# Kernel optimization log

Hardware: AMD Instinct MI355X
Metric: run time of the kernel (lower is better)

The kernel has to match this reference:

```python
import jax, jax.numpy as jnp
import numpy as np
from jax import lax

B, N, T = 64, 50, 30          # batch, history length, words per title
VOCAB, E = 50000, 300          # vocab size, word emb dim
FN, A, G, K = 400, 200, 400, 3 # filter_num, attention_dim, gru_unit, window size
USERS = 50000


def setup_inputs() -> dict:
    key = jax.random.key(0)
    ks = jax.random.split(key, 12)
    return {
        "user_id": jax.random.randint(ks[0], (B,), 0, USERS),
        "history_title": jax.random.randint(ks[1], (B, N, T), 0, VOCAB),
        "history_length": jax.random.randint(ks[2], (B,), 1, N + 1),
        "word_emb": jax.random.normal(ks[3], (VOCAB, E), jnp.float32) * 0.02,
        "conv_w": jax.random.normal(ks[4], (K, E, FN), jnp.float32) * 0.05,  # WIO layout
        "conv_b": jnp.zeros((FN,), jnp.float32),
        "v": jax.random.normal(ks[5], (FN, A), jnp.float32) * 0.05,
        "vb": jnp.zeros((A,), jnp.float32),
        "q": jax.random.normal(ks[6], (A, 1), jnp.float32) * 0.05,
        "user_emb": jax.random.normal(ks[7], (USERS, G), jnp.float32) * 0.02,
        "W_ih": jax.random.normal(ks[8], (3 * G, FN), jnp.float32) * 0.05,
        "W_hh": jax.random.normal(ks[9], (3 * G, G), jnp.float32) * 0.05,
        "b_ih": jnp.zeros((3 * G,), jnp.float32),
        "b_hh": jnp.zeros((3 * G,), jnp.float32),
    }


def _news_encode(history_title, word_emb, conv_w, conv_b, v, vb, q):
    # word embedding lookup: [B, N, T, E] (dropout is identity in eval mode)
    W = word_emb[history_title]
    # Conv1d over the word axis, padding=1 keeps length T
    x = W.reshape(B * N, T, E)
    C = lax.conv_general_dilated(
        x, conv_w, window_strides=(1,), padding=[(1, 1)],
        dimension_numbers=("NWC", "WIO", "NWC")) + conv_b
    C = jax.nn.relu(C).reshape(B, N, T, FN)
    # additive attention scores
    a = jnp.tanh(jnp.einsum("bntf,fa->bnta", C, v) + vb)
    a = jnp.einsum("bnta,ao->bnt", a, q)  # q: [A,1] -> squeeze
    # original uses Softmax(dim=0) on a [n, t] per sample => over the n-titles axis
    alpha = jax.nn.softmax(a, axis=1)
    # e[i] = alpha[i] @ C[i]: weighted sum over words -> [B, N, FN]
    return jnp.einsum("bnt,bntf->bnf", alpha, C)


def _gru(news_embed, h0, lengths, W_ih, W_hh, b_ih, b_hh):
    # packed_padded semantics: h stops updating once step >= length
    xs = jnp.swapaxes(news_embed, 0, 1)                 # [N, B, FN]
    mask = jnp.arange(N)[:, None] < lengths[None, :]    # [N, B]

    def step(h, inp):
        x_t, m = inp
        gx = x_t @ W_ih.T + b_ih                        # [B, 3G]
        gh = h @ W_hh.T + b_hh
        xr, xz, xn = jnp.split(gx, 3, axis=-1)
        hr, hz, hn = jnp.split(gh, 3, axis=-1)
        r = jax.nn.sigmoid(xr + hr)
        z = jax.nn.sigmoid(xz + hz)
        n = jnp.tanh(xn + r * hn)
        h_new = (1.0 - z) * n + z * h
        h = jnp.where(m[:, None], h_new, h)
        return h, None

    h_final, _ = lax.scan(step, h0, (xs, mask))
    return h_final


def reference(user_id, history_title, history_length, word_emb, conv_w, conv_b,
              v, vb, q, user_emb, W_ih, W_hh, b_ih, b_hh):
    news_embed = _news_encode(history_title, word_emb, conv_w, conv_b, v, vb, q)
    h0 = user_emb[user_id]                              # [B, G]
    return _gru(news_embed, h0, history_length, W_ih, W_hh, b_ih, b_hh)
```

## Files before the change

### kernel.cpp

```cpp
#include <hip/hip_runtime.h>
#include <hip/hip_bf16.h>

#define BB 64
#define NN 50
#define TT 30
#define EE 300
#define FN 400
#define AA 200
#define GG 400

typedef __attribute__((ext_vector_type(8))) short bf16x8;
typedef __attribute__((ext_vector_type(4))) float f32x4;

__device__ inline ushort f2bf(float x) {
  __hip_bfloat16 b = __float2bfloat16(x);
  return *(ushort*)&b;
}

__global__ void k_prep_all(
    const float* __restrict__ Whh, const float* __restrict__ cw,
    const float* __restrict__ v, const float* __restrict__ q,
    const float* __restrict__ vb, const float* __restrict__ Wih,
    const int* __restrict__ user_id, const float* __restrict__ user_emb,
    float* __restrict__ Wpack, __hip_bfloat16* __restrict__ WT2,
    __hip_bfloat16* __restrict__ vT, float* __restrict__ qp,
    float* __restrict__ vbp, __hip_bfloat16* __restrict__ Wih_bf,
    float* __restrict__ h0)
{
  int i = blockIdx.x * 256 + threadIdx.x;
  if (i < 480000) {
    int jl = i % 150;
    int g = (i / 150) % 400;
    int gc = i / 60000;
    int gate = jl / 50, gl = jl - gate * 50;
    int j = gate * 400 + gc * 50 + gl;
    Wpack[i] = Whh[j * 400 + g];
  } else if (i < 910080) {
    int k = i - 480000;
    int kk = k & 31, f = (k >> 5) % 448, s = k / (448 * 32);
    int ko = s / 10, e = (s - ko * 10) * 32 + kk;
    float val = (f < FN && e < EE) ? cw[(ko * EE + e) * FN + f] : 0.f;
    WT2[k] = __float2bfloat16(val);
  } else if (i < 1003264) {
    int k = i - 910080;
    int a = k / 416, f = k % 416;
    vT[k] = __float2bfloat16((a < AA && f < FN) ? v[f * AA + a] : 0.f);
  } else if (i < 1003488) {
    int k = i - 1003264;
    qp[k]  = k < AA ? q[k]  : 0.f;
    vbp[k] = k < AA ? vb[k] : 0.f;
  } else if (i < 1562592) {
    int k = i - 1003488;
    int j = k / 416, f = k % 416;
    Wih_bf[k] = __float2bfloat16((j < 1200 && f < FN) ? Wih[j * 400 + f] : 0.f);
  } else if (i < 1588192) {
    int k = i - 1562592;
    int b = k / GG, g = k - b * GG;
    h0[k] = user_emb[(size_t)user_id[b] * GG + g];
  }
}

__global__ __launch_bounds__(512, 4) void k_conv(
    const int* __restrict__ title, const float* __restrict__ word_emb,
    const __hip_bfloat16* __restrict__ WT2, const float* __restrict__ conv_b,
    __hip_bfloat16* __restrict__ C)
{
  __shared__ __align__(16) ushort E[2][34][340];
  __shared__ int words[60];
  const int g = blockIdx.x;
  const int tid = threadIdx.x;
  const int lane = tid & 63, wid = tid >> 6;
  const int ti = wid >> 2, wn = wid & 3;
  const int l15 = lane & 15, l4 = lane >> 4;

  if (tid < 60) words[tid] = title[g * 60 + tid];
  for (int idx = tid; idx < 2890; idx += 512)
    *(uint4*)((ushort*)E + idx * 8) = make_uint4(0u, 0u, 0u, 0u);
  __syncthreads();
  for (int idx = tid; idx < 4500; idx += 512) {
    int row = idx / 75, ch = idx - row * 75;
    int tt = row / 30, w = row - tt * 30;
    float4 v4 = *(const float4*)(word_emb + (size_t)words[row] * EE + ch * 4);
    ushort4 u4 = make_ushort4(f2bf(v4.x), f2bf(v4.y), f2bf(v4.z), f2bf(v4.w));
    *(ushort4*)(&E[tt][w + 1][ch * 4]) = u4;
  }
  __syncthreads();

  f32x4 acc[2][7];
#pragma unroll
  for (int nt = 0; nt < 7; ++nt) {
    int f = wn * 112 + nt * 16 + l15;
    float bj = (f < FN) ? conv_b[f] : 0.f;
#pragma unroll
    for (int mt = 0; mt < 2; ++mt) {
      acc[mt][nt][0] = bj; acc[mt][nt][1] = bj;
      acc[mt][nt][2] = bj; acc[mt][nt][3] = bj;
    }
  }

  const ushort* Bbase = (const ushort*)WT2 + (size_t)(wn * 112 + l15) * 32 + l4 * 8;

#pragma unroll
  for (int ko = 0; ko < 3; ++ko) {
#pragma unroll
    for (int ks = 0; ks < 10; ++ks) {
      const int s = ko * 10 + ks;
      bf16x8 bq[7];
#pragma unroll
      for (int nt = 0; nt < 7; ++nt)
        bq[nt] = *(const bf16x8*)(Bbase + (size_t)s * 14336 + nt * 512);
      bf16x8 af[2];
#pragma unroll
      for (int mt = 0; mt < 2; ++mt)
        af[mt] = *(const bf16x8*)(&E[ti][mt * 16 + l15 + ko][ks * 32 + l4 * 8]);
#pragma unroll
      for (int nt = 0; nt < 7; ++nt)
#pragma unroll
        for (int mt = 0; mt < 2; ++mt)
          acc[mt][nt] = __builtin_amdgcn_mfma_f32_16x16x32_bf16(af[mt], bq[nt], acc[mt][nt], 0, 0, 0);
    }
  }

#pragma unroll
  for (int mt = 0; mt < 2; ++mt) {
    int tb = mt * 16 + l4 * 4;
#pragma unroll
    for (int nt = 0; nt < 7; ++nt) {
      int f = wn * 112 + nt * 16 + l15;
      if (f < 416) {
#pragma unroll
        for (int r = 0; r < 4; ++r) {
          int t = tb + r;
          if (t < TT) {
            float vv = fmaxf(acc[mt][nt][r], 0.f);
            C[((size_t)(g * 2 + ti) * 30 + t) * 416 + f] = __float2bfloat16(vv);
          }
        }
      }
    }
  }
}

__global__ __launch_bounds__(512) void k_attn(
    const __hip_bfloat16* __restrict__ C, const __hip_bfloat16* __restrict__ vT,
    const float* __restrict__ vbp, const float* __restrict__ qp,
    float* __restrict__ score)
{
  __shared__ __align__(16) ushort Clds[256 * 40];
  __shared__ __align__(16) ushort Vlds[224 * 40];
  __shared__ float sred[2][256];
  const int tid = threadIdx.x;
  const int lane = tid & 63, wid = tid >> 6;
  const int wm = wid >> 1, wn = wid & 1;
  const int l15 = lane & 15, l4 = lane >> 4;
  const size_t row0 = (size_t)blockIdx.x * 256;

  f32x4 acc[4][7];
  float ql[7];
#pragma unroll
  for (int nt = 0; nt < 7; ++nt) {
    int a = wn * 112 + nt * 16 + l15;
    ql[nt] = qp[a];
    float vbv = vbp[a];
#pragma unroll
    for (int mt = 0; mt < 4; ++mt) {
      acc[mt][nt][0] = vbv; acc[mt][nt][1] = vbv;
      acc[mt][nt][2] = vbv; acc[mt][nt][3] = vbv;
    }
  }

  for (int ks = 0; ks < 13; ++ks) {
    for (int idx = tid; idx < 1024; idx += 512) {
      int r = idx >> 2, c = idx & 3;
      *(uint4*)(&Clds[r * 40 + c * 8]) =
          *(const uint4*)((const ushort*)C + (row0 + r) * 416 + ks * 32 + c * 8);
    }
    for (int idx = tid; idx < 896; idx += 512) {
      int a = idx >> 2, c = idx & 3;
      *(uint4*)(&Vlds[a * 40 + c * 8]) =
          *(const uint4*)((const ushort*)vT + a * 416 + ks * 32 + c * 8);
    }
    __syncthreads();
    bf16x8 cf[4];
#pragma unroll
    for (int mt = 0; mt < 4; ++mt)
      cf[mt] = *(const bf16x8*)(&Clds[(wm * 64 + mt * 16 + l15) * 40 + l4 * 8]);
#pragma unroll
    for (int nt = 0; nt < 7; ++nt) {
      bf16x8 vf = *(const bf16x8*)(&Vlds[(wn * 112 + nt * 16 + l15) * 40 + l4 * 8]);
#pragma unroll
      for (int mt = 0; mt < 4; ++mt)
        acc[mt][nt] = __builtin_amdgcn_mfma_f32_16x16x32_bf16(cf[mt], vf, acc[mt][nt], 0, 0, 0);
    }
    __syncthreads();
  }

  float sums[4][4];
#pragma unroll
  for (int mt = 0; mt < 4; ++mt)
#pragma unroll
    for (int r = 0; r < 4; ++r) sums[mt][r] = 0.f;
#pragma unroll
  for (int mt = 0; mt < 4; ++mt)
#pragma unroll
    for (int nt = 0; nt < 7; ++nt)
#pragma unroll
      for (int r = 0; r < 4; ++r)
        sums[mt][r] += tanhf(acc[mt][nt][r]) * ql[nt];
#pragma unroll
  for (int mask = 1; mask < 16; mask <<= 1)
#pragma unroll
    for (int mt = 0; mt < 4; ++mt)
#pragma unroll
      for (int r = 0; r < 4; ++r)
        sums[mt][r] += __shfl_xor(sums[mt][r], mask);

  float outv = 0.f;
#pragma unroll
  for (int mt = 0; mt < 4; ++mt)
#pragma unroll
    for (int r = 0; r < 4; ++r)
      if (l15 == mt * 4 + r) outv = sums[mt][r];
  sred[wn][wm * 64 + (l15 >> 2) * 16 + l4 * 4 + (l15 & 3)] = outv;
  __syncthreads();
  if (tid < 256) score[row0 + tid] = sred[0][tid] + sred[1][tid];
}

__global__ void k2_softmax_n(const float* __restrict__ score, float* __restrict__ alpha) {
  int i = blockIdx.x * 256 + threadIdx.x;
  if (i >= BB * TT) return;
  int b = i / TT, t = i - b * TT;
  int base = b * (NN * TT) + t;
  float m = -1e30f;
  for (int n = 0; n < NN; ++n) m = fmaxf(m, score[base + n * TT]);
  float s = 0.f;
  for (int n = 0; n < NN; ++n) s += __expf(score[base + n * TT] - m);
  float inv = 1.f / s;
  for (int n = 0; n < NN; ++n)
    alpha[base + n * TT] = __expf(score[base + n * TT] - m) * inv;
}

__global__ __launch_bounds__(256) void k3_wsum(
    const float* __restrict__ alpha, const __hip_bfloat16* __restrict__ C,
    __hip_bfloat16* __restrict__ Ebf) {
  __shared__ float al[TT];
  const int bn = blockIdx.x;
  const int tid = threadIdx.x;
  if (tid < TT) al[tid] = alpha[bn * TT + tid];
  __syncthreads();
  for (int f = tid; f < 416; f += 256) {
    float s = 0.f;
    if (f < FN) {
#pragma unroll
      for (int t = 0; t < TT; ++t)
        s = fmaf(al[t], __bfloat162float(C[((size_t)bn * TT + t) * 416 + f]), s);
    }
    Ebf[(size_t)bn * 416 + f] = __float2bfloat16(s);
  }
}

__global__ __launch_bounds__(512) void k4_gx_mfma(
    const __hip_bfloat16* __restrict__ Ebf,
    const __hip_bfloat16* __restrict__ Wih,
    const float* __restrict__ b_ih,
    float* __restrict__ gx)
{
  __shared__ __align__(16) ushort Alds[128 * 40];
  __shared__ __align__(16) ushort Blds[448 * 40];
  const int tid = threadIdx.x;
  const int lane = tid & 63, wid = tid >> 6;
  const int wm = wid >> 2, wn = wid & 3;
  const int l15 = lane & 15, l4 = lane >> 4;
  const int mb = blockIdx.x / 3;
  const int nb = blockIdx.x - mb * 3;
  const int row0 = mb * 128;
  const int n0 = nb * 448;

  f32x4 acc[4][7];
#pragma unroll
  for (int nt = 0; nt < 7; ++nt) {
    int j = n0 + wn * 112 + nt * 16 + l15;
    float bj = (j < 1200) ? b_ih[j] : 0.f;
#pragma unroll
    for (int mt = 0; mt < 4; ++mt) {
      acc[mt][nt][0] = bj; acc[mt][nt][1] = bj;
      acc[mt][nt][2] = bj; acc[mt][nt][3] = bj;
    }
  }

  const int ar = tid >> 2, ac = tid & 3;
  for (int ks = 0; ks < 13; ++ks) {
    *(uint4*)(&Alds[ar * 40 + ac * 8]) =
        *(const uint4*)((const ushort*)Ebf + (size_t)(row0 + ar) * 416 + ks * 32 + ac * 8);
    for (int idx = tid; idx < 1792; idx += 512) {
      int r = idx >> 2, c = idx & 3;
      *(uint4*)(&Blds[r * 40 + c * 8]) =
          *(const uint4*)((const ushort*)Wih + (size_t)(n0 + r) * 416 + ks * 32 + c * 8);
    }
    __syncthreads();
    bf16x8 af[4];
#pragma unroll
    for (int mt = 0; mt < 4; ++mt)
      af[mt] = *(const bf16x8*)(&Alds[(wm * 64 + mt * 16 + l15) * 40 + l4 * 8]);
#pragma unroll
    for (int nt = 0; nt < 7; ++nt) {
      bf16x8 bfr = *(const bf16x8*)(&Blds[(wn * 112 + nt * 16 + l15) * 40 + l4 * 8]);
#pragma unroll
      for (int mt = 0; mt < 4; ++mt)
        acc[mt][nt] = __builtin_amdgcn_mfma_f32_16x16x32_bf16(af[mt], bfr, acc[mt][nt], 0, 0, 0);
    }
    __syncthreads();
  }

#pragma unroll
  for (int mt = 0; mt < 4; ++mt) {
    int row = row0 + wm * 64 + mt * 16 + l4 * 4;
#pragma unroll
    for (int nt = 0; nt < 7; ++nt) {
      int j = n0 + wn * 112 + nt * 16 + l15;
      if (j < 1200) {
#pragma unroll
        for (int r = 0; r < 4; ++r)
          gx[(size_t)(row + r) * 1200 + j] = acc[mt][nt][r];
      }
    }
  }
}

__global__ __launch_bounds__(256) void k5_step(
    const float* __restrict__ h_prev, float* __restrict__ h_next,
    const float* __restrict__ Wpack, const float* __restrict__ b_hh,
    const float* __restrict__ gx, const int* __restrict__ hist_len,
    float* __restrict__ out, int step)
{
  const int gc = blockIdx.x & 7;
  const int bg = blockIdx.x >> 3;
  const int tid = threadIdx.x;
  __shared__ float hl[2][GG];
  __shared__ float ghl[2][3][50];

  for (int i = tid; i < 2 * GG; i += 256) {
    int b = i / GG, g = i - b * GG;
    hl[b][g] = h_prev[(2 * bg + b) * GG + g];
  }
  __syncthreads();

  if (tid < 150) {
    float a00 = 0.f, a01 = 0.f, a10 = 0.f, a11 = 0.f;
    const float* wp = Wpack + (size_t)gc * 60000 + tid;
#pragma unroll 4
    for (int g = 0; g < 200; ++g) {
      float w0 = wp[g * 150];
      float w1 = wp[(g + 200) * 150];
      a00 = fmaf(hl[0][g], w0, a00);
      a10 = fmaf(hl[1][g], w0, a10);
      a01 = fmaf(hl[0][g + 200], w1, a01);
      a11 = fmaf(hl[1][g + 200], w1, a11);
    }
    int gate = tid / 50, gl = tid - gate * 50;
    float bb = b_hh[gate * 400 + gc * 50 + gl];
    ghl[0][gate][gl] = a00 + a01 + bb;
    ghl[1][gate][gl] = a10 + a11 + bb;
  }
  __syncthreads();

  if (tid < 100) {
    int b = tid / 50, gl = tid - (tid / 50) * 50;
    int babs = 2 * bg + b;
    int g = gc * 50 + gl;
    const float* gxp = gx + ((size_t)babs * NN + step) * 1200;
    float xr = gxp[g], xz = gxp[400 + g], xn = gxp[800 + g];
    float hr = ghl[b][0][gl], hz = ghl[b][1][gl], hn = ghl[b][2][gl];
    float r = 1.f / (1.f + __expf(-(xr + hr)));
    float z = 1.f / (1.f + __expf(-(xz + hz)));
    float nv = tanhf(xn + r * hn);
    float hold = hl[b][g];
    float hnew = (1.f - z) * nv + z * hold;
    float hres = (step < hist_len[babs]) ? hnew : hold;
    h_next[babs * GG + g] = hres;
    if (step == NN - 1) out[babs * GG + g] = hres;
  }
}

extern "C" void kernel_launch(void* const* d_in, const int* in_sizes, int n_in,
                              void* d_out, int out_size, void* d_ws, size_t ws_size,
                              hipStream_t stream) {
  const int*   user_id   = (const int*)d_in[0];
  const int*   title     = (const int*)d_in[1];
  const int*   hist_len  = (const int*)d_in[2];
  const float* word_emb  = (const float*)d_in[3];
  const float* conv_w    = (const float*)d_in[4];
  const float* conv_b    = (const float*)d_in[5];
  const float* v         = (const float*)d_in[6];
  const float* vb        = (const float*)d_in[7];
  const float* q         = (const float*)d_in[8];
  const float* user_emb  = (const float*)d_in[9];
  const float* W_ih      = (const float*)d_in[10];
  const float* W_hh      = (const float*)d_in[11];
  const float* b_ih      = (const float*)d_in[12];
  const float* b_hh      = (const float*)d_in[13];
  float* out = (float*)d_out;

  char* ws = (char*)d_ws;
  size_t off = 0;
  auto take = [&](size_t bytes) {
    char* p = ws + off;
    off = (off + bytes + 255) & ~(size_t)255;
    return p;
  };
  __hip_bfloat16* C      = (__hip_bfloat16*)take((size_t)BB * NN * TT * 416 * 2);
  float* score  = (float*)take((size_t)BB * NN * TT * 4);
  float* alpha  = (float*)take((size_t)BB * NN * TT * 4);
  __hip_bfloat16* Ebf    = (__hip_bfloat16*)take((size_t)BB * NN * 416 * 2);
  __hip_bfloat16* Wih_bf = (__hip_bfloat16*)take((size_t)1344 * 416 * 2);
  float* Wpack  = (float*)take((size_t)8 * 400 * 150 * 4);
  float* gx     = (float*)take((size_t)BB * NN * 1200 * 4);
  float* h0     = (float*)take((size_t)BB * GG * 4);
  float* h1     = (float*)take((size_t)BB * GG * 4);
  __hip_bfloat16* WT2    = (__hip_bfloat16*)take((size_t)30 * 448 * 32 * 2);
  __hip_bfloat16* vT     = (__hip_bfloat16*)take((size_t)224 * 416 * 2);
  float* qp     = (float*)take(224 * 4);
  float* vbp    = (float*)take(224 * 4);
  (void)ws_size;

  k_prep_all<<<6204, 256, 0, stream>>>(W_hh, conv_w, v, q, vb, W_ih, user_id,
                                       user_emb, Wpack, WT2, vT, qp, vbp,
                                       Wih_bf, h0);

  k_conv<<<BB * NN / 2, 512, 0, stream>>>(title, word_emb, WT2, conv_b, C);
  k_attn<<<BB * NN * TT / 256, 512, 0, stream>>>(C, vT, vbp, qp, score);
  k2_softmax_n<<<(BB * TT + 255) / 256, 256, 0, stream>>>(score, alpha);
  k3_wsum<<<BB * NN, 256, 0, stream>>>(alpha, C, Ebf);
  k4_gx_mfma<<<75, 512, 0, stream>>>(Ebf, Wih_bf, b_ih, gx);

  float* hbuf[2] = {h0, h1};
  for (int step = 0; step < NN; ++step) {
    k5_step<<<256, 256, 0, stream>>>(hbuf[step & 1], hbuf[(step + 1) & 1],
                                     Wpack, b_hh, gx, hist_len, out, step);
  }
}
```

Measured before the change: 894.5 us.

## Reuse conv weight fragments across both titles and stream V weights directly from global

Result: no change. 882.0 us (-1.4%).

```diff
diff --git a/kernel.cpp b/kernel.cpp
--- a/kernel.cpp
+++ b/kernel.cpp
@@ -23,7 +23,7 @@
     const float* __restrict__ vb, const float* __restrict__ Wih,
     const int* __restrict__ user_id, const float* __restrict__ user_emb,
     float* __restrict__ Wpack, __hip_bfloat16* __restrict__ WT2,
-    __hip_bfloat16* __restrict__ vT, float* __restrict__ qp,
+    __hip_bfloat16* __restrict__ vT2, float* __restrict__ qp,
     float* __restrict__ vbp, __hip_bfloat16* __restrict__ Wih_bf,
     float* __restrict__ h0)
 {
@@ -43,8 +43,10 @@
     WT2[k] = __float2bfloat16(val);
   } else if (i < 1003264) {
     int k = i - 910080;
-    int a = k / 416, f = k % 416;
-    vT[k] = __float2bfloat16((a < AA && f < FN) ? v[f * AA + a] : 0.f);
+    int kk = k & 31, a = (k >> 5) % 224, ks = k / (224 * 32);
+    int e = ks * 32 + kk;
+    float val = (a < AA && e < FN) ? v[e * AA + a] : 0.f;
+    vT2[k] = __float2bfloat16(val);
   } else if (i < 1003488) {
     int k = i - 1003264;
     qp[k]  = k < AA ? q[k]  : 0.f;
@@ -60,24 +62,23 @@
   }
 }
 
-__global__ __launch_bounds__(512, 4) void k_conv(
+__global__ __launch_bounds__(256, 2) void k_conv(
     const int* __restrict__ title, const float* __restrict__ word_emb,
     const __hip_bfloat16* __restrict__ WT2, const float* __restrict__ conv_b,
     __hip_bfloat16* __restrict__ C)
 {
-  __shared__ __align__(16) ushort E[2][34][340];
+  __shared__ __align__(16) ushort E[2][34][344];
   __shared__ int words[60];
   const int g = blockIdx.x;
   const int tid = threadIdx.x;
-  const int lane = tid & 63, wid = tid >> 6;
-  const int ti = wid >> 2, wn = wid & 3;
+  const int lane = tid & 63, wn = tid >> 6;
   const int l15 = lane & 15, l4 = lane >> 4;
 
   if (tid < 60) words[tid] = title[g * 60 + tid];
-  for (int idx = tid; idx < 2890; idx += 512)
+  for (int idx = tid; idx < 2924; idx += 256)
     *(uint4*)((ushort*)E + idx * 8) = make_uint4(0u, 0u, 0u, 0u);
   __syncthreads();
-  for (int idx = tid; idx < 4500; idx += 512) {
+  for (int idx = tid; idx < 4500; idx += 256) {
     int row = idx / 75, ch = idx - row * 75;
     int tt = row / 30, w = row - tt * 30;
     float4 v4 = *(const float4*)(word_emb + (size_t)words[row] * EE + ch * 4);
@@ -86,13 +87,13 @@
   }
   __syncthreads();
 
-  f32x4 acc[2][7];
+  f32x4 acc[4][7];
 #pragma unroll
   for (int nt = 0; nt < 7; ++nt) {
     int f = wn * 112 + nt * 16 + l15;
     float bj = (f < FN) ? conv_b[f] : 0.f;
 #pragma unroll
-    for (int mt = 0; mt < 2; ++mt) {
+    for (int mt = 0; mt < 4; ++mt) {
       acc[mt][nt][0] = bj; acc[mt][nt][1] = bj;
       acc[mt][nt][2] = bj; acc[mt][nt][3] = bj;
     }
@@ -100,30 +101,43 @@
 
   const ushort* Bbase = (const ushort*)WT2 + (size_t)(wn * 112 + l15) * 32 + l4 * 8;
 
-#pragma unroll
-  for (int ko = 0; ko < 3; ++ko) {
-#pragma unroll
-    for (int ks = 0; ks < 10; ++ks) {
-      const int s = ko * 10 + ks;
-      bf16x8 bq[7];
-#pragma unroll
-      for (int nt = 0; nt < 7; ++nt)
-        bq[nt] = *(const bf16x8*)(Bbase + (size_t)s * 14336 + nt * 512);
-      bf16x8 af[2];
-#pragma unroll
-      for (int mt = 0; mt < 2; ++mt)
-        af[mt] = *(const bf16x8*)(&E[ti][mt * 16 + l15 + ko][ks * 32 + l4 * 8]);
-#pragma unroll
-      for (int nt = 0; nt < 7; ++nt)
-#pragma unroll
-        for (int mt = 0; mt < 2; ++mt)
-          acc[mt][nt] = __builtin_amdgcn_mfma_f32_16x16x32_bf16(af[mt], bq[nt], acc[mt][nt], 0, 0, 0);
-    }
-  }
-
-#pragma unroll
-  for (int mt = 0; mt < 2; ++mt) {
-    int tb = mt * 16 + l4 * 4;
+#define LOADB(dst, s) {                                                        \
+    const ushort* p_ = Bbase + (size_t)(s) * 14336;                            \
+    _Pragma("unroll")                                                          \
+    for (int nt = 0; nt < 7; ++nt) dst[nt] = *(const bf16x8*)(p_ + nt * 512);  \
+  }
+#define DOMFMA(bq, s) {                                                        \
+    const int ko_ = (s) / 10, ks_ = (s) % 10;                                  \
+    bf16x8 af_[4];                                                             \
+    _Pragma("unroll")                                                          \
+    for (int mt = 0; mt < 4; ++mt)                                             \
+      af_[mt] = *(const bf16x8*)(&E[mt >> 1][(mt & 1) * 16 + l15 + ko_]        \
+                                   [ks_ * 32 + l4 * 8]);                       \
+    _Pragma("unroll")                                                          \
+    for (int nt = 0; nt < 7; ++nt)                                             \
+      _Pragma("unroll")                                                        \
+      for (int mt = 0; mt < 4; ++mt)                                           \
+        acc[mt][nt] = __builtin_amdgcn_mfma_f32_16x16x32_bf16(                 \
+            af_[mt], bq[nt], acc[mt][nt], 0, 0, 0);                            \
+  }
+
+  bf16x8 bqA[7], bqB[7];
+  LOADB(bqA, 0);
+#pragma unroll
+  for (int it = 0; it < 15; ++it) {
+    const int s0 = it * 2;
+    LOADB(bqB, s0 + 1);
+    DOMFMA(bqA, s0);
+    if (it < 14) LOADB(bqA, s0 + 2);
+    DOMFMA(bqB, s0 + 1);
+  }
+#undef LOADB
+#undef DOMFMA
+
+#pragma unroll
+  for (int mt = 0; mt < 4; ++mt) {
+    const int ti = mt >> 1;
+    const int tb = (mt & 1) * 16 + l4 * 4;
 #pragma unroll
     for (int nt = 0; nt < 7; ++nt) {
       int f = wn * 112 + nt * 16 + l15;
@@ -142,12 +156,11 @@
 }
 
 __global__ __launch_bounds__(512) void k_attn(
-    const __hip_bfloat16* __restrict__ C, const __hip_bfloat16* __restrict__ vT,
+    const __hip_bfloat16* __restrict__ C, const __hip_bfloat16* __restrict__ vT2,
     const float* __restrict__ vbp, const float* __restrict__ qp,
     float* __restrict__ score)
 {
   __shared__ __align__(16) ushort Clds[256 * 40];
-  __shared__ __align__(16) ushort Vlds[224 * 40];
   __shared__ float sred[2][256];
   const int tid = threadIdx.x;
   const int lane = tid & 63, wid = tid >> 6;
@@ -169,29 +182,28 @@
     }
   }
 
+  const ushort* Vbase = (const ushort*)vT2 + (size_t)(wn * 112 + l15) * 32 + l4 * 8;
+
   for (int ks = 0; ks < 13; ++ks) {
+    bf16x8 vf[7];
+#pragma unroll
+    for (int nt = 0; nt < 7; ++nt)
+      vf[nt] = *(const bf16x8*)(Vbase + ((size_t)ks * 224 + nt * 16) * 32);
     for (int idx = tid; idx < 1024; idx += 512) {
       int r = idx >> 2, c = idx & 3;
       *(uint4*)(&Clds[r * 40 + c * 8]) =
           *(const uint4*)((const ushort*)C + (row0 + r) * 416 + ks * 32 + c * 8);
     }
-    for (int idx = tid; idx < 896; idx += 512) {
-      int a = idx >> 2, c = idx & 3;
-      *(uint4*)(&Vlds[a * 40 + c * 8]) =
-          *(const uint4*)((const ushort*)vT + a * 416 + ks * 32 + c * 8);
-    }
     __syncthreads();
     bf16x8 cf[4];
 #pragma unroll
     for (int mt = 0; mt < 4; ++mt)
       cf[mt] = *(const bf16x8*)(&Clds[(wm * 64 + mt * 16 + l15) * 40 + l4 * 8]);
 #pragma unroll
-    for (int nt = 0; nt < 7; ++nt) {
-      bf16x8 vf = *(const bf16x8*)(&Vlds[(wn * 112 + nt * 16 + l15) * 40 + l4 * 8]);
+    for (int nt = 0; nt < 7; ++nt)
 #pragma unroll
       for (int mt = 0; mt < 4; ++mt)
-        acc[mt][nt] = __builtin_amdgcn_mfma_f32_16x16x32_bf16(cf[mt], vf, acc[mt][nt], 0, 0, 0);
-    }
+        acc[mt][nt] = __builtin_amdgcn_mfma_f32_16x16x32_bf16(cf[mt], vf[nt], acc[mt][nt], 0, 0, 0);
     __syncthreads();
   }
 
@@ -418,17 +430,17 @@
   float* h0     = (float*)take((size_t)BB * GG * 4);
   float* h1     = (float*)take((size_t)BB * GG * 4);
   __hip_bfloat16* WT2    = (__hip_bfloat16*)take((size_t)30 * 448 * 32 * 2);
-  __hip_bfloat16* vT     = (__hip_bfloat16*)take((size_t)224 * 416 * 2);
+  __hip_bfloat16* vT2    = (__hip_bfloat16*)take((size_t)13 * 224 * 32 * 2);
   float* qp     = (float*)take(224 * 4);
   float* vbp    = (float*)take(224 * 4);
   (void)ws_size;
 
   k_prep_all<<<6204, 256, 0, stream>>>(W_hh, conv_w, v, q, vb, W_ih, user_id,
-                                       user_emb, Wpack, WT2, vT, qp, vbp,
+                                       user_emb, Wpack, WT2, vT2, qp, vbp,
                                        Wih_bf, h0);
 
-  k_conv<<<BB * NN / 2, 512, 0, stream>>>(title, word_emb, WT2, conv_b, C);
-  k_attn<<<BB * NN * TT / 256, 512, 0, stream>>>(C, vT, vbp, qp, score);
+  k_conv<<<BB * NN / 2, 256, 0, stream>>>(title, word_emb, WT2, conv_b, C);
+  k_attn<<<BB * NN * TT / 256, 512, 0, stream>>>(C, vT2, vbp, qp, score);
   k2_softmax_n<<<(BB * TT + 255) / 256, 256, 0, stream>>>(score, alpha);
   k3_wsum<<<BB * NN, 256, 0, stream>>>(alpha, C, Ebf);
   k4_gx_mfma<<<75, 512, 0, stream>>>(Ebf, Wih_bf, b_ih, gx);
```
